# Kernel optimization log

Hardware: AMD Instinct MI355X
Metric: run time of the kernel (lower is better)

## Reference

```python
import jax, jax.numpy as jnp
import numpy as np

N_NODES = 50000
N_EDGES = 800000
D = 128            # in_channels == hidden_channels
N_LAYERS = 3
OUT = 16
N_GRAPHS = 128


def setup_inputs() -> dict:
    key = jax.random.key(0)
    ks = jax.random.split(key, 12)
    x = jax.random.normal(ks[0], (N_NODES, D), dtype=jnp.float32)
    edge_index = jax.random.randint(ks[1], (2, N_EDGES), 0, N_NODES, dtype=jnp.int64)
    batch_ids = jnp.sort(jax.random.randint(ks[2], (N_NODES,), 0, N_GRAPHS, dtype=jnp.int64))
    s = 1.0 / np.sqrt(D)
    # Stacked per-layer GraphConv weights (all layers are D->D here).
    Wrel = jax.random.uniform(ks[3], (N_LAYERS, D, D), jnp.float32, -s, s)
    brel = jax.random.uniform(ks[4], (N_LAYERS, D), jnp.float32, -s, s)
    Wroot = jax.random.uniform(ks[5], (N_LAYERS, D, D), jnp.float32, -s, s)
    # post_mp MLP head
    W1 = jax.random.uniform(ks[6], (D, D), jnp.float32, -s, s)
    b1 = jax.random.uniform(ks[7], (D,), jnp.float32, -s, s)
    W2 = jax.random.uniform(ks[8], (D, OUT), jnp.float32, -s, s)
    b2 = jax.random.uniform(ks[9], (OUT,), jnp.float32, -s, s)
    return {"x": x, "edge_index": edge_index, "batch_ids": batch_ids,
            "Wrel": Wrel, "brel": brel, "Wroot": Wroot,
            "W1": W1, "b1": b1, "W2": W2, "b2": b2}


def reference(x, edge_index, batch_ids, Wrel, brel, Wroot, W1, b1, W2, b2):
    src, dst = edge_index[0], edge_index[1]
    h = x
    for l in range(N_LAYERS):
        # GraphConv: lin_rel(sum_{j->i} h_j) + lin_root(h_i)
        agg = jax.ops.segment_sum(h[src], dst, num_segments=N_NODES)  # [N, D]
        h = agg @ Wrel[l] + brel[l] + h @ Wroot[l]
        h = jax.nn.relu(h)
        # dropout p=0.0 / eval mode -> identity
    # global mean pool over graphs
    sums = jax.ops.segment_sum(h, batch_ids, num_segments=N_GRAPHS)          # [G, D]
    counts = jax.ops.segment_sum(jnp.ones((N_NODES,), h.dtype), batch_ids,
                                 num_segments=N_GRAPHS)                       # [G]
    pooled = sums / jnp.maximum(counts, 1.0)[:, None]
    # post_mp MLP (dropout identity in eval)
    out = (pooled @ W1 + b1) @ W2 + b2                                        # [G, OUT]
    return out
```

## Files before the change

kernel.cpp:

```cpp
#include <hip/hip_runtime.h>

#define N_NODES 50000
#define N_EDGES 800000
#define D 128
#define N_LAYERS 3
#define OUT_F 16
#define N_GRAPHS 128
#define NBUCK 391
#define EPB 4096
#define NB3 ((N_EDGES + EPB - 1) / EPB)
#define CAP 4096
#define NT32 ((N_NODES + 31) / 32)
#define NGB4 ((NT32 + 3) / 4)
#define NCAST 6250
#define NPREPW 96

typedef __attribute__((ext_vector_type(8))) short short8;
typedef __attribute__((ext_vector_type(16))) float floatx16;

__device__ __forceinline__ unsigned short f2bf(float f) {
  unsigned int u = __float_as_uint(f);
  u += 0x7fff + ((u >> 16) & 1);
  return (unsigned short)(u >> 16);
}
__device__ __forceinline__ float bf2f(unsigned short b) {
  return __uint_as_float(((unsigned int)b) << 16);
}
__device__ __forceinline__ float blo(unsigned v) { return __uint_as_float(v << 16); }
__device__ __forceinline__ float bhi(unsigned v) { return __uint_as_float(v & 0xffff0000u); }

__global__ __launch_bounds__(256) void partition_kernel(
    const int* __restrict__ src, const int* __restrict__ dst,
    int* __restrict__ cursor, unsigned* __restrict__ pairs) {
  __shared__ unsigned pk[EPB];
  __shared__ int hist[NBUCK];
  __shared__ int wcur[NBUCK];
  const int e0 = blockIdx.x * EPB;
  const int n = min(EPB, N_EDGES - e0);
  const int t = threadIdx.x;
  for (int i = t; i < NBUCK; i += 256) hist[i] = 0;
  __syncthreads();
  for (int i = t; i < n; i += 256) {
    int d = dst[e0 + i], s = src[e0 + i];
    pk[i] = ((unsigned)d << 16) | (unsigned)s;
    atomicAdd(&hist[d >> 7], 1);
  }
  __syncthreads();
  for (int i = t; i < NBUCK; i += 256)
    wcur[i] = i * CAP + (hist[i] ? atomicAdd(&cursor[i], hist[i]) : 0);
  __syncthreads();
  for (int i = t; i < n; i += 256) {
    unsigned p = pk[i];
    int pos = atomicAdd(&wcur[p >> 23], 1);
    pairs[pos] = p;
  }
}

__global__ __launch_bounds__(256) void bucket_sort_kernel(
    const unsigned* __restrict__ pairs, const int* __restrict__ cursor,
    int* __restrict__ rowbeg, int* __restrict__ rowend, int* __restrict__ esrc) {
  __shared__ unsigned pk[CAP];
  __shared__ int sorted[CAP];
  __shared__ int hist[128], off[128], cur[128];
  const int bkt = blockIdx.x;
  const int t = threadIdx.x;
  const int beg = bkt * CAP;
  const int cnt = cursor[bkt];
  if (t < 128) hist[t] = 0;
  __syncthreads();
  for (int i = t; i < cnt; i += 256) {
    unsigned p = pairs[beg + i];
    pk[i] = p;
    atomicAdd(&hist[(p >> 16) & 127], 1);
  }
  __syncthreads();
  if (t < 128) off[t] = hist[t];
  __syncthreads();
  for (int o = 1; o < 128; o <<= 1) {
    int x = (t < 128 && t >= o) ? off[t - o] : 0;
    __syncthreads();
    if (t < 128) off[t] += x;
    __syncthreads();
  }
  if (t < 128) {
    int node = bkt * 128 + t;
    if (node < N_NODES) {
      rowbeg[node] = beg + off[t] - hist[t];
      rowend[node] = beg + off[t];
    }
    cur[t] = off[t] - hist[t];
  }
  __syncthreads();
  for (int i = t; i < cnt; i += 256) {
    unsigned p = pk[i];
    int pos = atomicAdd(&cur[(p >> 16) & 127], 1);
    sorted[pos] = (int)(p & 0xFFFFu);
  }
  __syncthreads();
  for (int i = t; i < cnt; i += 256) esrc[beg + i] = sorted[i];
}

__global__ __launch_bounds__(256) void prep_all_kernel(
    const float* __restrict__ x, unsigned short* __restrict__ x16,
    const float* __restrict__ Wrel, const float* __restrict__ Wroot,
    unsigned short* __restrict__ wt, int* __restrict__ cursor) {
  const int bid = blockIdx.x;
  const int t = threadIdx.x;
  if (bid < NCAST) {
    const int i = bid * 256 + t;
    const float4 v = *(const float4*)&x[(size_t)i * 4];
    uint2 o;
    o.x = f2bf(v.x) | ((unsigned)f2bf(v.y) << 16);
    o.y = f2bf(v.z) | ((unsigned)f2bf(v.w) << 16);
    *(uint2*)&x16[(size_t)i * 4] = o;
  } else if (bid < NCAST + NPREPW) {
    const int idx = (bid - NCAST) * 256 + t;
    const int lane = idx & 63;
    const int kst = (idx >> 6) & 31;
    const int nt = (idx >> 11) & 1;
    const int half = (idx >> 12) & 1;
    const int l = idx >> 13;
    const int n = half * 64 + nt * 32 + (lane & 31);
    const int kx0 = kst * 16 + (lane >> 5) * 8;
    const int seg = kx0 >> 7;
    const int k0 = kx0 & 127;
    const int mat = seg >> 1, lo = seg & 1;
    const float* W = (mat ? Wroot : Wrel) + (size_t)l * D * D;
    unsigned short v[8];
#pragma unroll
    for (int j = 0; j < 8; ++j) {
      float w = W[(size_t)(k0 + j) * D + n];
      unsigned short hi = f2bf(w);
      v[j] = lo ? f2bf(w - bf2f(hi)) : hi;
    }
    unsigned short* dstp =
        wt + ((size_t)l * 128 + (half * 2 + nt) * 32 + kst) * 512 + lane * 8;
    *(uint4*)dstp = *(const uint4*)v;
  } else {
    const int i = (bid - NCAST - NPREPW) * 256 + t;
    if (i < NBUCK) cursor[i] = 0;
  }
}

__global__ __launch_bounds__(256) void agg_kernel(
    const unsigned short* __restrict__ h,
    const int* __restrict__ rowbeg, const int* __restrict__ rowend,
    const int* __restrict__ esrc, unsigned short* __restrict__ agg) {
  const int idx = blockIdx.x * 256 + threadIdx.x;
  const int n = idx >> 4;
  const int lane = idx & 15;
  if (n >= N_NODES) return;
  const int beg = rowbeg[n], end = rowend[n];
  float a0 = 0, a1 = 0, a2 = 0, a3 = 0, a4 = 0, a5 = 0, a6 = 0, a7 = 0;
  int e = beg;
  for (; e + 4 <= end; e += 4) {
    const int s0 = esrc[e],     s1 = esrc[e + 1];
    const int s2 = esrc[e + 2], s3 = esrc[e + 3];
    const uint4 v0 = *(const uint4*)&h[(size_t)s0 * D + lane * 8];
    const uint4 v1 = *(const uint4*)&h[(size_t)s1 * D + lane * 8];
    const uint4 v2 = *(const uint4*)&h[(size_t)s2 * D + lane * 8];
    const uint4 v3 = *(const uint4*)&h[(size_t)s3 * D + lane * 8];
    a0 += blo(v0.x) + blo(v1.x) + blo(v2.x) + blo(v3.x);
    a1 += bhi(v0.x) + bhi(v1.x) + bhi(v2.x) + bhi(v3.x);
    a2 += blo(v0.y) + blo(v1.y) + blo(v2.y) + blo(v3.y);
    a3 += bhi(v0.y) + bhi(v1.y) + bhi(v2.y) + bhi(v3.y);
    a4 += blo(v0.z) + blo(v1.z) + blo(v2.z) + blo(v3.z);
    a5 += bhi(v0.z) + bhi(v1.z) + bhi(v2.z) + bhi(v3.z);
    a6 += blo(v0.w) + blo(v1.w) + blo(v2.w) + blo(v3.w);
    a7 += bhi(v0.w) + bhi(v1.w) + bhi(v2.w) + bhi(v3.w);
  }
  for (; e < end; ++e) {
    const int s0 = esrc[e];
    const uint4 v0 = *(const uint4*)&h[(size_t)s0 * D + lane * 8];
    a0 += blo(v0.x); a1 += bhi(v0.x);
    a2 += blo(v0.y); a3 += bhi(v0.y);
    a4 += blo(v0.z); a5 += bhi(v0.z);
    a6 += blo(v0.w); a7 += bhi(v0.w);
  }
  uint4 o;
  o.x = f2bf(a0) | ((unsigned)f2bf(a1) << 16);
  o.y = f2bf(a2) | ((unsigned)f2bf(a3) << 16);
  o.z = f2bf(a4) | ((unsigned)f2bf(a5) << 16);
  o.w = f2bf(a6) | ((unsigned)f2bf(a7) << 16);
  *(uint4*)&agg[(size_t)n * D + lane * 8] = o;
}

__global__ __launch_bounds__(256, 2) void gemm_kernel(
    const unsigned short* __restrict__ agg, const unsigned short* __restrict__ hv,
    const unsigned short* __restrict__ wt,
    const float* __restrict__ brel,
    unsigned short* __restrict__ outp) {
  __shared__ unsigned short blds[32768];
  const int t = threadIdx.x;
  const int wave = t >> 6, lane = t & 63;
  const int r2 = lane & 31, hseg = lane >> 5;
  const int tile = blockIdx.x * 4 + wave;
  const int r0 = tile * 32;
  int arow = r0 + r2;
  if (arow >= N_NODES) arow = N_NODES - 1;

  short8 ag[8], hh[8];
  const unsigned short* ap = agg + (size_t)arow * D + hseg * 8;
  const unsigned short* hp = hv + (size_t)arow * D + hseg * 8;
#pragma unroll
  for (int i = 0; i < 8; ++i) {
    ag[i] = *(const short8*)(ap + i * 16);
    hh[i] = *(const short8*)(hp + i * 16);
  }

#pragma unroll
  for (int pp = 0; pp < 2; ++pp) {
    if (pp) __syncthreads();
    const unsigned short* ws = wt + (size_t)pp * 32768;
#pragma unroll
    for (int j = 0; j < 16; ++j) {
      const int idx = t + j * 256;
      *(uint4*)&blds[idx * 8] = *(const uint4*)&ws[idx * 8];
    }
    __syncthreads();
#pragma unroll
    for (int p2 = 0; p2 < 2; ++p2) {
      floatx16 acc = {0.f};
#pragma unroll
      for (int kst = 0; kst < 32; ++kst) {
        const short8 af = (kst < 16) ? ag[kst & 7] : hh[kst & 7];
        const short8 b = *(const short8*)&blds[(p2 * 32 + kst) * 512 + lane * 8];
        acc = __builtin_amdgcn_mfma_f32_32x32x16_bf16(af, b, acc, 0, 0, 0);
      }
      const int cb = (pp * 2 + p2) * 32 + r2;
      const float bias = brel[cb];
#pragma unroll
      for (int reg = 0; reg < 16; ++reg) {
        const int orow = r0 + (reg & 3) + 8 * (reg >> 2) + 4 * hseg;
        if (orow < N_NODES)
          outp[(size_t)orow * D + cb] = f2bf(fmaxf(acc[reg] + bias, 0.f));
      }
    }
  }
}

__device__ __forceinline__ int lb_search(const int* __restrict__ a, int n, int key) {
  int lo = 0, hi = n;
  while (lo < hi) {
    int m = (lo + hi) >> 1;
    if (a[m] < key) lo = m + 1; else hi = m;
  }
  return lo;
}

__global__ __launch_bounds__(256) void pool_head_kernel(
    const unsigned short* __restrict__ h, const int* __restrict__ batch,
    const float* __restrict__ W1, const float* __restrict__ b1,
    const float* __restrict__ W2, const float* __restrict__ b2,
    float* __restrict__ out) {
  __shared__ float sums_lds[16][128];
  __shared__ float pooled[128];
  __shared__ float hidden[128];
  __shared__ int range[2];
  const int g = blockIdx.x;
  const int t = threadIdx.x;
  if (t < 2) range[t] = lb_search(batch, N_NODES, g + t);
  __syncthreads();
  const int lo = range[0], hi = range[1];
  const int rg = t >> 4, cg = t & 15;
  float a0 = 0, a1 = 0, a2 = 0, a3 = 0, a4 = 0, a5 = 0, a6 = 0, a7 = 0;
  for (int n = lo + rg; n < hi; n += 16) {
    const uint4 v = *(const uint4*)&h[(size_t)n * D + cg * 8];
    a0 += blo(v.x); a1 += bhi(v.x);
    a2 += blo(v.y); a3 += bhi(v.y);
    a4 += blo(v.z); a5 += bhi(v.z);
    a6 += blo(v.w); a7 += bhi(v.w);
  }
  sums_lds[rg][cg * 8 + 0] = a0; sums_lds[rg][cg * 8 + 1] = a1;
  sums_lds[rg][cg * 8 + 2] = a2; sums_lds[rg][cg * 8 + 3] = a3;
  sums_lds[rg][cg * 8 + 4] = a4; sums_lds[rg][cg * 8 + 5] = a5;
  sums_lds[rg][cg * 8 + 6] = a6; sums_lds[rg][cg * 8 + 7] = a7;
  __syncthreads();
  if (t < 128) {
    float s = 0.f;
#pragma unroll
    for (int r = 0; r < 16; ++r) s += sums_lds[r][t];
    pooled[t] = s / fmaxf((float)(hi - lo), 1.f);
  }
  __syncthreads();
  if (t < 128) {
    float a = b1[t];
    for (int k = 0; k < D; ++k) a += pooled[k] * W1[k * D + t];
    hidden[t] = a;
  }
  __syncthreads();
  if (t < OUT_F) {
    float o = b2[t];
    for (int k = 0; k < D; ++k) o += hidden[k] * W2[k * OUT_F + t];
    out[(size_t)g * OUT_F + t] = o;
  }
}

extern "C" void kernel_launch(void* const* d_in, const int* in_sizes, int n_in,
                              void* d_out, int out_size, void* d_ws, size_t ws_size,
                              hipStream_t stream) {
  const float* x     = (const float*)d_in[0];
  const int*   ei    = (const int*)d_in[1];
  const int*   batch = (const int*)d_in[2];
  const float* Wrel  = (const float*)d_in[3];
  const float* brel  = (const float*)d_in[4];
  const float* Wroot = (const float*)d_in[5];
  const float* W1    = (const float*)d_in[6];
  const float* b1    = (const float*)d_in[7];
  const float* W2    = (const float*)d_in[8];
  const float* b2    = (const float*)d_in[9];
  float* out = (float*)d_out;

  const size_t ND = (size_t)N_NODES * D;
  unsigned short* bufA = (unsigned short*)d_ws;
  unsigned short* bufB = bufA + ND;
  unsigned short* bufC = bufB + ND;
  unsigned short* wt   = bufC + ND;
  int* rowbeg = (int*)(wt + (size_t)N_LAYERS * 128 * 512);
  int* rowend = rowbeg + N_NODES;
  int* esrc   = rowend + N_NODES;
  unsigned* pairs = (unsigned*)(esrc + (size_t)NBUCK * CAP);
  int* cursor = (int*)(pairs + (size_t)NBUCK * CAP);

  const int* esrc_in = ei;
  const int* edst_in = ei + N_EDGES;

  prep_all_kernel<<<NCAST + NPREPW + 2, 256, 0, stream>>>(
      x, bufC, Wrel, Wroot, wt, cursor);
  partition_kernel<<<NB3, 256, 0, stream>>>(esrc_in, edst_in, cursor, pairs);
  bucket_sort_kernel<<<NBUCK, 256, 0, stream>>>(pairs, cursor, rowbeg, rowend, esrc);

  const size_t WL = (size_t)128 * 512;
  const int agg_blocks = (N_NODES * 16 + 255) / 256;
  agg_kernel<<<agg_blocks, 256, 0, stream>>>(bufC, rowbeg, rowend, esrc, bufB);
  gemm_kernel<<<NGB4, 256, 0, stream>>>(bufB, bufC, wt, brel, bufA);
  agg_kernel<<<agg_blocks, 256, 0, stream>>>(bufA, rowbeg, rowend, esrc, bufB);
  gemm_kernel<<<NGB4, 256, 0, stream>>>(bufB, bufA, wt + WL, brel + D, bufC);
  agg_kernel<<<agg_blocks, 256, 0, stream>>>(bufC, rowbeg, rowend, esrc, bufB);
  gemm_kernel<<<NGB4, 256, 0, stream>>>(bufB, bufC, wt + 2 * WL, brel + 2 * D, bufA);

  pool_head_kernel<<<N_GRAPHS, 256, 0, stream>>>(bufA, batch, W1, b1, W2, b2, out);
}
```

Baseline: 274.1 us.

## Merge partition into prep kernel, remap agg blocks, widen GEMM blocks

```diff
diff --git a/kernel.cpp b/kernel.cpp
--- a/kernel.cpp
+++ b/kernel.cpp
@@ -11,7 +11,8 @@
 #define NB3 ((N_EDGES + EPB - 1) / EPB)
 #define CAP 4096
 #define NT32 ((N_NODES + 31) / 32)
-#define NGB4 ((NT32 + 3) / 4)
+#define NUNIT 196
+#define NAGGC 400
 #define NCAST 6250
 #define NPREPW 96
 
@@ -29,92 +30,45 @@
 __device__ __forceinline__ float blo(unsigned v) { return __uint_as_float(v << 16); }
 __device__ __forceinline__ float bhi(unsigned v) { return __uint_as_float(v & 0xffff0000u); }
 
-__global__ __launch_bounds__(256) void partition_kernel(
+__global__ __launch_bounds__(256) void prep_part_kernel(
     const int* __restrict__ src, const int* __restrict__ dst,
-    int* __restrict__ cursor, unsigned* __restrict__ pairs) {
+    int* __restrict__ cursor, unsigned* __restrict__ pairs,
+    const float* __restrict__ x, unsigned short* __restrict__ x16,
+    const float* __restrict__ Wrel, const float* __restrict__ Wroot,
+    unsigned short* __restrict__ wt) {
   __shared__ unsigned pk[EPB];
   __shared__ int hist[NBUCK];
   __shared__ int wcur[NBUCK];
-  const int e0 = blockIdx.x * EPB;
-  const int n = min(EPB, N_EDGES - e0);
-  const int t = threadIdx.x;
-  for (int i = t; i < NBUCK; i += 256) hist[i] = 0;
-  __syncthreads();
-  for (int i = t; i < n; i += 256) {
-    int d = dst[e0 + i], s = src[e0 + i];
-    pk[i] = ((unsigned)d << 16) | (unsigned)s;
-    atomicAdd(&hist[d >> 7], 1);
-  }
-  __syncthreads();
-  for (int i = t; i < NBUCK; i += 256)
-    wcur[i] = i * CAP + (hist[i] ? atomicAdd(&cursor[i], hist[i]) : 0);
-  __syncthreads();
-  for (int i = t; i < n; i += 256) {
-    unsigned p = pk[i];
-    int pos = atomicAdd(&wcur[p >> 23], 1);
-    pairs[pos] = p;
-  }
-}
-
-__global__ __launch_bounds__(256) void bucket_sort_kernel(
-    const unsigned* __restrict__ pairs, const int* __restrict__ cursor,
-    int* __restrict__ rowbeg, int* __restrict__ rowend, int* __restrict__ esrc) {
-  __shared__ unsigned pk[CAP];
-  __shared__ int sorted[CAP];
-  __shared__ int hist[128], off[128], cur[128];
-  const int bkt = blockIdx.x;
-  const int t = threadIdx.x;
-  const int beg = bkt * CAP;
-  const int cnt = cursor[bkt];
-  if (t < 128) hist[t] = 0;
-  __syncthreads();
-  for (int i = t; i < cnt; i += 256) {
-    unsigned p = pairs[beg + i];
-    pk[i] = p;
-    atomicAdd(&hist[(p >> 16) & 127], 1);
-  }
-  __syncthreads();
-  if (t < 128) off[t] = hist[t];
-  __syncthreads();
-  for (int o = 1; o < 128; o <<= 1) {
-    int x = (t < 128 && t >= o) ? off[t - o] : 0;
-    __syncthreads();
-    if (t < 128) off[t] += x;
-    __syncthreads();
-  }
-  if (t < 128) {
-    int node = bkt * 128 + t;
-    if (node < N_NODES) {
-      rowbeg[node] = beg + off[t] - hist[t];
-      rowend[node] = beg + off[t];
-    }
-    cur[t] = off[t] - hist[t];
-  }
-  __syncthreads();
-  for (int i = t; i < cnt; i += 256) {
-    unsigned p = pk[i];
-    int pos = atomicAdd(&cur[(p >> 16) & 127], 1);
-    sorted[pos] = (int)(p & 0xFFFFu);
-  }
-  __syncthreads();
-  for (int i = t; i < cnt; i += 256) esrc[beg + i] = sorted[i];
-}
-
-__global__ __launch_bounds__(256) void prep_all_kernel(
-    const float* __restrict__ x, unsigned short* __restrict__ x16,
-    const float* __restrict__ Wrel, const float* __restrict__ Wroot,
-    unsigned short* __restrict__ wt, int* __restrict__ cursor) {
   const int bid = blockIdx.x;
   const int t = threadIdx.x;
-  if (bid < NCAST) {
-    const int i = bid * 256 + t;
+  if (bid < NB3) {
+    const int e0 = bid * EPB;
+    const int n = min(EPB, N_EDGES - e0);
+    for (int i = t; i < NBUCK; i += 256) hist[i] = 0;
+    __syncthreads();
+    for (int i = t; i < n; i += 256) {
+      int d = dst[e0 + i], s = src[e0 + i];
+      pk[i] = ((unsigned)d << 16) | (unsigned)s;
+      atomicAdd(&hist[d >> 7], 1);
+    }
+    __syncthreads();
+    for (int i = t; i < NBUCK; i += 256)
+      wcur[i] = i * CAP + (hist[i] ? atomicAdd(&cursor[i], hist[i]) : 0);
+    __syncthreads();
+    for (int i = t; i < n; i += 256) {
+      unsigned p = pk[i];
+      int pos = atomicAdd(&wcur[p >> 23], 1);
+      pairs[pos] = p;
+    }
+  } else if (bid < NB3 + NCAST) {
+    const int i = (bid - NB3) * 256 + t;
     const float4 v = *(const float4*)&x[(size_t)i * 4];
     uint2 o;
     o.x = f2bf(v.x) | ((unsigned)f2bf(v.y) << 16);
     o.y = f2bf(v.z) | ((unsigned)f2bf(v.w) << 16);
     *(uint2*)&x16[(size_t)i * 4] = o;
-  } else if (bid < NCAST + NPREPW) {
-    const int idx = (bid - NCAST) * 256 + t;
+  } else {
+    const int idx = (bid - NB3 - NCAST) * 256 + t;
     const int lane = idx & 63;
     const int kst = (idx >> 6) & 31;
     const int nt = (idx >> 11) & 1;
@@ -136,19 +90,64 @@
     unsigned short* dstp =
         wt + ((size_t)l * 128 + (half * 2 + nt) * 32 + kst) * 512 + lane * 8;
     *(uint4*)dstp = *(const uint4*)v;
-  } else {
-    const int i = (bid - NCAST - NPREPW) * 256 + t;
-    if (i < NBUCK) cursor[i] = 0;
-  }
+  }
+}
+
+__global__ __launch_bounds__(256) void bucket_sort_kernel(
+    const unsigned* __restrict__ pairs, const int* __restrict__ cursor,
+    int* __restrict__ rowbeg, int* __restrict__ rowend, int* __restrict__ esrc) {
+  __shared__ unsigned pk[CAP];
+  __shared__ int sorted[CAP];
+  __shared__ int hist[128], off[128], cur[128];
+  const int bkt = blockIdx.x;
+  const int t = threadIdx.x;
+  const int beg = bkt * CAP;
+  const int cnt = cursor[bkt];
+  if (t < 128) hist[t] = 0;
+  __syncthreads();
+  for (int i = t; i < cnt; i += 256) {
+    unsigned p = pairs[beg + i];
+    pk[i] = p;
+    atomicAdd(&hist[(p >> 16) & 127], 1);
+  }
+  __syncthreads();
+  if (t < 128) off[t] = hist[t];
+  __syncthreads();
+  for (int o = 1; o < 128; o <<= 1) {
+    int x = (t < 128 && t >= o) ? off[t - o] : 0;
+    __syncthreads();
+    if (t < 128) off[t] += x;
+    __syncthreads();
+  }
+  if (t < 128) {
+    int node = bkt * 128 + t;
+    if (node < N_NODES) {
+      rowbeg[node] = beg + off[t] - hist[t];
+      rowend[node] = beg + off[t];
+    }
+    cur[t] = off[t] - hist[t];
+  }
+  __syncthreads();
+  for (int i = t; i < cnt; i += 256) {
+    unsigned p = pk[i];
+    int pos = atomicAdd(&cur[(p >> 16) & 127], 1);
+    sorted[pos] = (int)(p & 0xFFFFu);
+  }
+  __syncthreads();
+  for (int i = t; i < cnt; i += 256) esrc[beg + i] = sorted[i];
 }
 
 __global__ __launch_bounds__(256) void agg_kernel(
     const unsigned short* __restrict__ h,
     const int* __restrict__ rowbeg, const int* __restrict__ rowend,
     const int* __restrict__ esrc, unsigned short* __restrict__ agg) {
-  const int idx = blockIdx.x * 256 + threadIdx.x;
-  const int n = idx >> 4;
-  const int lane = idx & 15;
+  const int bid = blockIdx.x;
+  const int x = bid & 7, s = bid >> 3;
+  const int t = threadIdx.x;
+  const int c = s * 16 + (t >> 4);
+  const int u = x + 8 * (c >> 8);
+  const int n = u * 256 + (c & 255);
+  const int lane = t & 15;
   if (n >= N_NODES) return;
   const int beg = rowbeg[n], end = rowend[n];
   float a0 = 0, a1 = 0, a2 = 0, a3 = 0, a4 = 0, a5 = 0, a6 = 0, a7 = 0;
@@ -185,7 +184,7 @@
   *(uint4*)&agg[(size_t)n * D + lane * 8] = o;
 }
 
-__global__ __launch_bounds__(256, 2) void gemm_kernel(
+__global__ __launch_bounds__(512, 2) void gemm_kernel(
     const unsigned short* __restrict__ agg, const unsigned short* __restrict__ hv,
     const unsigned short* __restrict__ wt,
     const float* __restrict__ brel,
@@ -194,7 +193,7 @@
   const int t = threadIdx.x;
   const int wave = t >> 6, lane = t & 63;
   const int r2 = lane & 31, hseg = lane >> 5;
-  const int tile = blockIdx.x * 4 + wave;
+  const int tile = blockIdx.x * 8 + wave;
   const int r0 = tile * 32;
   int arow = r0 + r2;
   if (arow >= N_NODES) arow = N_NODES - 1;
@@ -213,8 +212,8 @@
     if (pp) __syncthreads();
     const unsigned short* ws = wt + (size_t)pp * 32768;
 #pragma unroll
-    for (int j = 0; j < 16; ++j) {
-      const int idx = t + j * 256;
+    for (int j = 0; j < 8; ++j) {
+      const int idx = t + j * 512;
       *(uint4*)&blds[idx * 8] = *(const uint4*)&ws[idx * 8];
     }
     __syncthreads();
@@ -325,19 +324,19 @@
   const int* esrc_in = ei;
   const int* edst_in = ei + N_EDGES;
 
-  prep_all_kernel<<<NCAST + NPREPW + 2, 256, 0, stream>>>(
-      x, bufC, Wrel, Wroot, wt, cursor);
-  partition_kernel<<<NB3, 256, 0, stream>>>(esrc_in, edst_in, cursor, pairs);
+  hipMemsetAsync(cursor, 0, NBUCK * sizeof(int), stream);
+  prep_part_kernel<<<NB3 + NCAST + NPREPW, 256, 0, stream>>>(
+      esrc_in, edst_in, cursor, pairs, x, bufC, Wrel, Wroot, wt);
   bucket_sort_kernel<<<NBUCK, 256, 0, stream>>>(pairs, cursor, rowbeg, rowend, esrc);
 
   const size_t WL = (size_t)128 * 512;
-  const int agg_blocks = (N_NODES * 16 + 255) / 256;
+  const int agg_blocks = 8 * NAGGC;
   agg_kernel<<<agg_blocks, 256, 0, stream>>>(bufC, rowbeg, rowend, esrc, bufB);
-  gemm_kernel<<<NGB4, 256, 0, stream>>>(bufB, bufC, wt, brel, bufA);
+  gemm_kernel<<<NUNIT, 512, 0, stream>>>(bufB, bufC, wt, brel, bufA);
   agg_kernel<<<agg_blocks, 256, 0, stream>>>(bufA, rowbeg, rowend, esrc, bufB);
-  gemm_kernel<<<NGB4, 256, 0, stream>>>(bufB, bufA, wt + WL, brel + D, bufC);
+  gemm_kernel<<<NUNIT, 512, 0, stream>>>(bufB, bufA, wt + WL, brel + D, bufC);
   agg_kernel<<<agg_blocks, 256, 0, stream>>>(bufC, rowbeg, rowend, esrc, bufB);
-  gemm_kernel<<<NGB4, 256, 0, stream>>>(bufB, bufC, wt + 2 * WL, brel + 2 * D, bufA);
+  gemm_kernel<<<NUNIT, 512, 0, stream>>>(bufB, bufC, wt + 2 * WL, brel + 2 * D, bufA);
 
   pool_head_kernel<<<N_GRAPHS, 256, 0, stream>>>(bufA, batch, W1, b1, W2, b2, out);
 }
```

After: 268.7 us. -2.0%, faster.
